# Kernel tuning notes

Hardware: AMD Instinct MI355X
Metric: run time of the kernel (lower is better)

The kernel has to match this reference:

```python
import jax, jax.numpy as jnp
import numpy as np

K = 5  # neighbors per node


def build_knn_adjacency(x, k=K):
    # x: (B, N, D) -> adj: (B, N, N)
    B, N, D = x.shape
    x_norm = x / jnp.clip(jnp.linalg.norm(x, axis=-1, keepdims=True), 1e-12)
    sim = jnp.einsum('bnd,bmd->bnm', x_norm, x_norm)  # (B, N, N)
    eye = jnp.eye(N, dtype=bool)
    sim = jnp.where(eye[None], jnp.asarray(-1.0, sim.dtype), sim)
    _, knn_idx = jax.lax.top_k(sim, k)  # (B, N, k)
    b_ix = jnp.arange(B)[:, None, None]
    i_ix = jnp.arange(N)[None, :, None]
    adj = jnp.zeros((B, N, N), dtype=x.dtype).at[b_ix, i_ix, knn_idx].set(1.0)
    adj = adj + jnp.eye(N, dtype=x.dtype)[None]
    return adj


def gcn_layer(x, adj, W, b):
    # deg-normalized aggregation then linear (torch Linear: x @ W.T + b)
    deg = adj.sum(axis=-1, keepdims=True)
    adj_norm = adj / jnp.clip(deg, 1.0)
    out = jnp.einsum('bnm,bmd->bnd', adj_norm, x)
    return out @ W.T + b


def setup_inputs() -> dict:
    key = jax.random.key(0)
    k1, k2, k3, k4, k5 = jax.random.split(key, 5)
    B, N, D, H = 32, 1024, 128, 128
    scale = 1.0 / np.sqrt(D)
    return {
        'x': jax.random.normal(k1, (B, N, D), dtype=jnp.float32),
        'W1': jax.random.normal(k2, (H, D), dtype=jnp.float32) * scale,
        'b1': jax.random.normal(k3, (H,), dtype=jnp.float32) * 0.01,
        'W2': jax.random.normal(k4, (H, H), dtype=jnp.float32) * scale,
        'b2': jax.random.normal(k5, (H,), dtype=jnp.float32) * 0.01,
    }


def reference(x, W1, b1, W2, b2):
    adj = build_knn_adjacency(x, k=K)
    h = x + jax.nn.relu(gcn_layer(x, adj, W1, b1))
    h = h + jax.nn.relu(gcn_layer(h, adj, W2, b2))
    return h  # pool='none' -> (B, N, hidden_dim)
```

## Files before the change

kernel.cpp:

```cpp
#include <hip/hip_runtime.h>
#include <float.h>
#include <math.h>

#define BB 32
#define NN 1024
#define DD 128
#define KK 5

typedef __attribute__((ext_vector_type(8))) short bf16x8;
typedef __attribute__((ext_vector_type(4))) float f32x4;

__device__ __forceinline__ unsigned short f2bf(float f) {
    unsigned int u = __float_as_uint(f);
    return (unsigned short)((u + 0x7FFFu + ((u >> 16) & 1u)) >> 16);
}
__device__ __forceinline__ float bf2f(unsigned short h) {
    return __uint_as_float(((unsigned int)h) << 16);
}

__global__ __launch_bounds__(256) void k_norm(const float* __restrict__ x,
                                              unsigned short* __restrict__ ph,
                                              unsigned short* __restrict__ pm,
                                              unsigned short* __restrict__ pl) {
    int row  = blockIdx.x * 4 + (threadIdx.x >> 6);
    int lane = threadIdx.x & 63;
    float2 v = *reinterpret_cast<const float2*>(x + (size_t)row * DD + lane * 2);
    float ss = v.x * v.x + v.y * v.y;
#pragma unroll
    for (int o = 32; o >= 1; o >>= 1) ss += __shfl_xor(ss, o);
    float inv = 1.0f / fmaxf(sqrtf(ss), 1e-12f);
    float y0 = v.x * inv, y1 = v.y * inv;

    unsigned short h0 = f2bf(y0);             float r0 = y0 - bf2f(h0);
    unsigned short m0 = f2bf(r0);             float s0 = r0 - bf2f(m0);
    unsigned short l0 = f2bf(s0);
    unsigned short h1 = f2bf(y1);             float r1 = y1 - bf2f(h1);
    unsigned short m1 = f2bf(r1);             float s1 = r1 - bf2f(m1);
    unsigned short l1 = f2bf(s1);

    size_t o = (size_t)row * DD + lane * 2;
    *reinterpret_cast<unsigned int*>(ph + o) = (unsigned int)h0 | ((unsigned int)h1 << 16);
    *reinterpret_cast<unsigned int*>(pm + o) = (unsigned int)m0 | ((unsigned int)m1 << 16);
    *reinterpret_cast<unsigned int*>(pl + o) = (unsigned int)l0 | ((unsigned int)l1 << 16);
}

__device__ __forceinline__ void stage_plane(const unsigned short* __restrict__ g,
                                            unsigned short (*s)[40], int tid,
                                            size_t rowbase, int c) {
#pragma unroll
    for (int hh = 0; hh < 2; ++hh) {
        int u = tid + (hh << 8);
        int row = u >> 2, q = u & 3;
        const float4 v = *reinterpret_cast<const float4*>(
            g + (rowbase + row) * DD + (c << 5) + (q << 3));
        *reinterpret_cast<float4*>(&s[row][q << 3]) = v;
    }
}

__global__ __launch_bounds__(256, 2) void k_sim(const unsigned short* __restrict__ ph,
                                                const unsigned short* __restrict__ pm,
                                                const unsigned short* __restrict__ pl,
                                                float* __restrict__ sim, int b0) {
    int t  = blockIdx.x;
    int bl = t / 36;
    int p  = t - bl * 36;
    int ti = 0;
    while (p >= 8 - ti) { p -= 8 - ti; ++ti; }
    int tj = ti + p;
    int R  = ti << 7, Cc = tj << 7;

    __shared__ unsigned short Ah[128][40], Am[128][40], Al[128][40];
    __shared__ unsigned short Bh[128][40], Bm[128][40], Bl[128][40];

    int tid  = threadIdx.x;
    int wv   = tid >> 6;
    int lane = tid & 63;
    int wr = (wv >> 1) << 6;
    int wc = (wv & 1) << 6;

    size_t base  = (size_t)(b0 + bl) * NN;
    size_t rbA = base + R, rbB = base + Cc;

    f32x4 acc[4][4];
#pragma unroll
    for (int i = 0; i < 4; ++i)
#pragma unroll
        for (int j = 0; j < 4; ++j) acc[i][j] = (f32x4){0.f, 0.f, 0.f, 0.f};

    int kk = (lane >> 4) << 3;
    int fr = lane & 15;

    for (int c = 0; c < 4; ++c) {
        if (c) __syncthreads();
        stage_plane(ph, Ah, tid, rbA, c);
        stage_plane(pm, Am, tid, rbA, c);
        stage_plane(pl, Al, tid, rbA, c);
        stage_plane(ph, Bh, tid, rbB, c);
        stage_plane(pm, Bm, tid, rbB, c);
        stage_plane(pl, Bl, tid, rbB, c);
        __syncthreads();

        bf16x8 bh[4], bm[4], blo[4];
#pragma unroll
        for (int cp = 0; cp < 4; ++cp) {
            int rb = wc + cp * 16 + fr;
            bh[cp]  = *reinterpret_cast<const bf16x8*>(&Bh[rb][kk]);
            bm[cp]  = *reinterpret_cast<const bf16x8*>(&Bm[rb][kk]);
            blo[cp] = *reinterpret_cast<const bf16x8*>(&Bl[rb][kk]);
        }
#pragma unroll
        for (int rp = 0; rp < 4; ++rp) {
            int ra = wr + rp * 16 + fr;
            bf16x8 ah = *reinterpret_cast<const bf16x8*>(&Ah[ra][kk]);
            bf16x8 am = *reinterpret_cast<const bf16x8*>(&Am[ra][kk]);
            bf16x8 al = *reinterpret_cast<const bf16x8*>(&Al[ra][kk]);
#pragma unroll
            for (int cp = 0; cp < 4; ++cp) {
                f32x4 cacc = acc[rp][cp];
                cacc = __builtin_amdgcn_mfma_f32_16x16x32_bf16(ah, bh[cp],  cacc, 0, 0, 0);
                cacc = __builtin_amdgcn_mfma_f32_16x16x32_bf16(ah, bm[cp],  cacc, 0, 0, 0);
                cacc = __builtin_amdgcn_mfma_f32_16x16x32_bf16(am, bh[cp],  cacc, 0, 0, 0);
                cacc = __builtin_amdgcn_mfma_f32_16x16x32_bf16(ah, blo[cp], cacc, 0, 0, 0);
                cacc = __builtin_amdgcn_mfma_f32_16x16x32_bf16(al, bh[cp],  cacc, 0, 0, 0);
                cacc = __builtin_amdgcn_mfma_f32_16x16x32_bf16(am, bm[cp],  cacc, 0, 0, 0);
                acc[rp][cp] = cacc;
            }
        }
    }

    float* Cb = sim + (size_t)bl * NN * NN;
    int crow = R + wr + ((lane >> 4) << 2);
    int ccol = Cc + wc + fr;
#pragma unroll
    for (int rp = 0; rp < 4; ++rp)
#pragma unroll
        for (int reg = 0; reg < 4; ++reg) {
            size_t rowo = (size_t)(crow + rp * 16 + reg) * NN + ccol;
#pragma unroll
            for (int cp = 0; cp < 4; ++cp)
                Cb[rowo + cp * 16] = acc[rp][cp][reg];
        }
    if (ti != tj) {
#pragma unroll
        for (int cp = 0; cp < 4; ++cp) {
            size_t mr = (size_t)(Cc + wc + cp * 16 + fr) * NN + (R + wr + ((lane >> 4) << 2));
#pragma unroll
            for (int rp = 0; rp < 4; ++rp)
                *reinterpret_cast<float4*>(&Cb[mr + rp * 16]) =
                    make_float4(acc[rp][cp][0], acc[rp][cp][1], acc[rp][cp][2], acc[rp][cp][3]);
        }
    }
}

__global__ __launch_bounds__(256) void k_topk(const float* __restrict__ sim,
                                              int* __restrict__ idx, int b0) {
    int lrow = blockIdx.x * 4 + (threadIdx.x >> 6);
    int lane = threadIdx.x & 63;
    const float* sr = sim + (size_t)lrow * NN;
    int i = lrow & (NN - 1);

    float v[16];
#pragma unroll
    for (int q = 0; q < 4; ++q) {
        float4 f = *reinterpret_cast<const float4*>(sr + lane * 16 + q * 4);
        v[q * 4 + 0] = f.x; v[q * 4 + 1] = f.y; v[q * 4 + 2] = f.z; v[q * 4 + 3] = f.w;
    }
    if ((i >> 4) == lane) {
        int s = i & 15;
#pragma unroll
        for (int j = 0; j < 16; ++j) if (j == s) v[j] = -FLT_MAX;
    }
    int* op = idx + ((size_t)b0 * NN + lrow) * KK;
#pragma unroll
    for (int t = 0; t < KK; ++t) {
        float bv = v[0]; int bj = 0;
#pragma unroll
        for (int j = 1; j < 16; ++j) if (v[j] > bv) { bv = v[j]; bj = j; }
        int bm = (lane << 4) + bj;
#pragma unroll
        for (int o = 1; o < 64; o <<= 1) {
            float ov = __shfl_xor(bv, o);
            int   om = __shfl_xor(bm, o);
            if (ov > bv || (ov == bv && om < bm)) { bv = ov; bm = om; }
        }
        if ((bm >> 4) == lane) {
            int s = bm & 15;
#pragma unroll
            for (int j = 0; j < 16; ++j) if (j == s) v[j] = -FLT_MAX;
        }
        if (lane == 0) op[t] = bm;
    }
}

#define SW(c) ((c) + 4 * ((c) >> 5))
#define LDW 140

__global__ __launch_bounds__(256, 3) void k_gcn(const float* __restrict__ h,
                                                const int* __restrict__ idx,
                                                const float* __restrict__ W,
                                                const float* __restrict__ bias,
                                                const float* __restrict__ res,
                                                float* __restrict__ out) {
    int rt = blockIdx.x << 6;
    __shared__ float As[64][68];
    __shared__ float Bs[64][LDW];
    int tid = threadIdx.x;
    int tr  = (tid >> 4) << 2;
    int tc  = (tid & 15) << 3;
    int stc = SW(tc);

    float acc[4][8];
#pragma unroll
    for (int i = 0; i < 4; ++i)
#pragma unroll
        for (int j = 0; j < 8; ++j) acc[i][j] = 0.f;

#pragma unroll
    for (int kc = 0; kc < 2; ++kc) {
        if (kc) __syncthreads();
        {
            int kv = tid & 15, r0 = tid >> 4;
            int colf = (kc << 6) + (kv << 2);
#pragma unroll
            for (int p = 0; p < 4; ++p) {
                int lrow = r0 + (p << 4);
                int grow = rt + lrow;
                const int* ip = idx + (size_t)grow * KK;
                const float* hb = h + (((size_t)grow >> 10) << 10) * DD;
                float4 v = *reinterpret_cast<const float4*>(h + (size_t)grow * DD + colf);
#pragma unroll
                for (int t = 0; t < KK; ++t) {
                    const float4 u = *reinterpret_cast<const float4*>(hb + (size_t)ip[t] * DD + colf);
                    v.x += u.x; v.y += u.y; v.z += u.z; v.w += u.w;
                }
                const float c = 1.0f / 6.0f;
                int k = kv << 2;
                As[k + 0][lrow] = v.x * c; As[k + 1][lrow] = v.y * c;
                As[k + 2][lrow] = v.z * c; As[k + 3][lrow] = v.w * c;
            }
        }
        {
            int kv = tid & 15, r0 = tid >> 4;
            const float* g = W + kc * 64;
#pragma unroll
            for (int p = 0; p < 8; ++p) {
                int r = r0 + (p << 4);
                const float4 v = *reinterpret_cast<const float4*>(g + (size_t)r * DD + (kv << 2));
                int k = kv << 2, row = SW(r);
                Bs[k + 0][row] = v.x; Bs[k + 1][row] = v.y;
                Bs[k + 2][row] = v.z; Bs[k + 3][row] = v.w;
            }
        }
        __syncthreads();
#pragma unroll 4
        for (int k = 0; k < 64; ++k) {
            const float4 a  = *reinterpret_cast<const float4*>(&As[k][tr]);
            const float4 b0 = *reinterpret_cast<const float4*>(&Bs[k][stc]);
            const float4 b1 = *reinterpret_cast<const float4*>(&Bs[k][stc + 4]);
            const float av[4] = {a.x, a.y, a.z, a.w};
            const float bw[8] = {b0.x, b0.y, b0.z, b0.w, b1.x, b1.y, b1.z, b1.w};
#pragma unroll
            for (int ii = 0; ii < 4; ++ii)
#pragma unroll
                for (int jj = 0; jj < 8; ++jj)
                    acc[ii][jj] = fmaf(av[ii], bw[jj], acc[ii][jj]);
        }
    }
    const float4 bz0 = *reinterpret_cast<const float4*>(bias + tc);
    const float4 bz1 = *reinterpret_cast<const float4*>(bias + tc + 4);
    const float bb[8] = {bz0.x, bz0.y, bz0.z, bz0.w, bz1.x, bz1.y, bz1.z, bz1.w};
#pragma unroll
    for (int i = 0; i < 4; ++i) {
        size_t ro = (size_t)(rt + tr + i) * DD + tc;
        const float4 r0 = *reinterpret_cast<const float4*>(res + ro);
        const float4 r1 = *reinterpret_cast<const float4*>(res + ro + 4);
        float4 o0, o1;
        o0.x = r0.x + fmaxf(acc[i][0] + bb[0], 0.f);
        o0.y = r0.y + fmaxf(acc[i][1] + bb[1], 0.f);
        o0.z = r0.z + fmaxf(acc[i][2] + bb[2], 0.f);
        o0.w = r0.w + fmaxf(acc[i][3] + bb[3], 0.f);
        o1.x = r1.x + fmaxf(acc[i][4] + bb[4], 0.f);
        o1.y = r1.y + fmaxf(acc[i][5] + bb[5], 0.f);
        o1.z = r1.z + fmaxf(acc[i][6] + bb[6], 0.f);
        o1.w = r1.w + fmaxf(acc[i][7] + bb[7], 0.f);
        *reinterpret_cast<float4*>(out + ro)     = o0;
        *reinterpret_cast<float4*>(out + ro + 4) = o1;
    }
}

extern "C" void kernel_launch(void* const* d_in, const int* in_sizes, int n_in,
                              void* d_out, int out_size, void* d_ws, size_t ws_size,
                              hipStream_t stream) {
    const float* x  = (const float*)d_in[0];
    const float* W1 = (const float*)d_in[1];
    const float* b1 = (const float*)d_in[2];
    const float* W2 = (const float*)d_in[3];
    const float* b2 = (const float*)d_in[4];
    float* out = (float*)d_out;

    char* ws = (char*)d_ws;
    size_t pl_b  = (size_t)BB * NN * DD * 2;
    size_t h1_b  = (size_t)BB * NN * DD * 4;
    size_t idx_b = (size_t)BB * NN * KK * 4;
    unsigned short* ph = (unsigned short*)ws;  ws += pl_b;
    unsigned short* pm = (unsigned short*)ws;  ws += pl_b;
    unsigned short* pl = (unsigned short*)ws;  ws += pl_b;
    float* h1  = (float*)ws;                   ws += h1_b;
    int*   idx = (int*)ws;                     ws += idx_b;
    float* sim = (float*)ws;
    size_t fixed = 3 * pl_b + h1_b + idx_b;
    size_t sim_avail = (ws_size > fixed) ? (ws_size - fixed) : 0;
    int SB = (int)(sim_avail / ((size_t)NN * NN * 4));
    if (SB > BB) SB = BB;
    if (SB < 1) SB = 1;

    k_norm<<<BB * NN / 4, 256, 0, stream>>>(x, ph, pm, pl);
    for (int b0 = 0; b0 < BB; b0 += SB) {
        int sb = (SB < BB - b0) ? SB : (BB - b0);
        k_sim<<<sb * 36, 256, 0, stream>>>(ph, pm, pl, sim, b0);
        k_topk<<<sb * NN / 4, 256, 0, stream>>>(sim, idx, b0);
    }
    k_gcn<<<BB * NN / 64, 256, 0, stream>>>(x,  idx, W1, b1, x,  h1);
    k_gcn<<<BB * NN / 64, 256, 0, stream>>>(h1, idx, W2, b2, h1, out);
}
```

Measured before the change: 172.1 us.

## Stage sim output through LDS, remap blocks, and restructure GCN gather

The similarity kernel now writes its output tile through shared memory (a union with the staging buffers), so both the direct and the mirrored tiles are stored as coalesced float4 rows instead of scattered scalar stores. Block IDs are remapped across the 8 XCDs. The batch-chunk loop is dropped and the full sim buffer is assumed to fit in the workspace, which could overflow if the workspace is smaller. The GCN kernel gathers the whole 64x128 aggregated tile once up front with row-major float4 loads and then streams W in four 32-wide chunks, trading a larger LDS footprint for fewer redundant gathers.

```diff
diff --git a/kernel.cpp b/kernel.cpp
--- a/kernel.cpp
+++ b/kernel.cpp
@@ -44,41 +44,50 @@
     *reinterpret_cast<unsigned int*>(pl + o) = (unsigned int)l0 | ((unsigned int)l1 << 16);
 }
 
+union SMem {
+    struct {
+        unsigned short Ah[128][40], Am[128][40], Al[128][40];
+        unsigned short Bh[128][40], Bm[128][40], Bl[128][40];
+    } s;
+    float q[4][32][68];
+};
+
 __device__ __forceinline__ void stage_plane(const unsigned short* __restrict__ g,
                                             unsigned short (*s)[40], int tid,
                                             size_t rowbase, int c) {
 #pragma unroll
     for (int hh = 0; hh < 2; ++hh) {
         int u = tid + (hh << 8);
-        int row = u >> 2, q = u & 3;
+        int row = u >> 2, qq = u & 3;
         const float4 v = *reinterpret_cast<const float4*>(
-            g + (rowbase + row) * DD + (c << 5) + (q << 3));
-        *reinterpret_cast<float4*>(&s[row][q << 3]) = v;
+            g + (rowbase + row) * DD + (c << 5) + (qq << 3));
+        *reinterpret_cast<float4*>(&s[row][qq << 3]) = v;
     }
 }
 
 __global__ __launch_bounds__(256, 2) void k_sim(const unsigned short* __restrict__ ph,
                                                 const unsigned short* __restrict__ pm,
                                                 const unsigned short* __restrict__ pl,
-                                                float* __restrict__ sim, int b0) {
-    int t  = blockIdx.x;
-    int bl = t / 36;
-    int p  = t - bl * 36;
+                                                float* __restrict__ sim) {
+    int bid = blockIdx.x;
+    int lb  = (bid & 7) * 144 + (bid >> 3);
+    int bl  = lb / 36;
+    int p   = lb - bl * 36;
     int ti = 0;
     while (p >= 8 - ti) { p -= 8 - ti; ++ti; }
     int tj = ti + p;
     int R  = ti << 7, Cc = tj << 7;
 
-    __shared__ unsigned short Ah[128][40], Am[128][40], Al[128][40];
-    __shared__ unsigned short Bh[128][40], Bm[128][40], Bl[128][40];
+    __shared__ SMem sm;
 
     int tid  = threadIdx.x;
     int wv   = tid >> 6;
     int lane = tid & 63;
     int wr = (wv >> 1) << 6;
     int wc = (wv & 1) << 6;
-
-    size_t base  = (size_t)(b0 + bl) * NN;
+    int lg = lane >> 4, fr = lane & 15;
+
+    size_t base = (size_t)bl * NN;
     size_t rbA = base + R, rbB = base + Cc;
 
     f32x4 acc[4][4];
@@ -87,33 +96,32 @@
 #pragma unroll
         for (int j = 0; j < 4; ++j) acc[i][j] = (f32x4){0.f, 0.f, 0.f, 0.f};
 
-    int kk = (lane >> 4) << 3;
-    int fr = lane & 15;
+    int kk = lg << 3;
 
     for (int c = 0; c < 4; ++c) {
         if (c) __syncthreads();
-        stage_plane(ph, Ah, tid, rbA, c);
-        stage_plane(pm, Am, tid, rbA, c);
-        stage_plane(pl, Al, tid, rbA, c);
-        stage_plane(ph, Bh, tid, rbB, c);
-        stage_plane(pm, Bm, tid, rbB, c);
-        stage_plane(pl, Bl, tid, rbB, c);
+        stage_plane(ph, sm.s.Ah, tid, rbA, c);
+        stage_plane(pm, sm.s.Am, tid, rbA, c);
+        stage_plane(pl, sm.s.Al, tid, rbA, c);
+        stage_plane(ph, sm.s.Bh, tid, rbB, c);
+        stage_plane(pm, sm.s.Bm, tid, rbB, c);
+        stage_plane(pl, sm.s.Bl, tid, rbB, c);
         __syncthreads();
 
         bf16x8 bh[4], bm[4], blo[4];
 #pragma unroll
         for (int cp = 0; cp < 4; ++cp) {
             int rb = wc + cp * 16 + fr;
-            bh[cp]  = *reinterpret_cast<const bf16x8*>(&Bh[rb][kk]);
-            bm[cp]  = *reinterpret_cast<const bf16x8*>(&Bm[rb][kk]);
-            blo[cp] = *reinterpret_cast<const bf16x8*>(&Bl[rb][kk]);
+            bh[cp]  = *reinterpret_cast<const bf16x8*>(&sm.s.Bh[rb][kk]);
+            bm[cp]  = *reinterpret_cast<const bf16x8*>(&sm.s.Bm[rb][kk]);
+            blo[cp] = *reinterpret_cast<const bf16x8*>(&sm.s.Bl[rb][kk]);
         }
 #pragma unroll
         for (int rp = 0; rp < 4; ++rp) {
             int ra = wr + rp * 16 + fr;
-            bf16x8 ah = *reinterpret_cast<const bf16x8*>(&Ah[ra][kk]);
-            bf16x8 am = *reinterpret_cast<const bf16x8*>(&Am[ra][kk]);
-            bf16x8 al = *reinterpret_cast<const bf16x8*>(&Al[ra][kk]);
+            bf16x8 ah = *reinterpret_cast<const bf16x8*>(&sm.s.Ah[ra][kk]);
+            bf16x8 am = *reinterpret_cast<const bf16x8*>(&sm.s.Am[ra][kk]);
+            bf16x8 al = *reinterpret_cast<const bf16x8*>(&sm.s.Al[ra][kk]);
 #pragma unroll
             for (int cp = 0; cp < 4; ++cp) {
                 f32x4 cacc = acc[rp][cp];
@@ -128,32 +136,51 @@
         }
     }
 
-    float* Cb = sim + (size_t)bl * NN * NN;
-    int crow = R + wr + ((lane >> 4) << 2);
-    int ccol = Cc + wc + fr;
-#pragma unroll
-    for (int rp = 0; rp < 4; ++rp)
-#pragma unroll
-        for (int reg = 0; reg < 4; ++reg) {
-            size_t rowo = (size_t)(crow + rp * 16 + reg) * NN + ccol;
+    __syncthreads();
+    float (*q)[68] = sm.q[wv];
+    float* Cb = sim + base * NN;
+
+    if (ti != tj) {
+#pragma unroll
+        for (int hp = 0; hp < 2; ++hp) {
+#pragma unroll
+            for (int rp = 0; rp < 4; ++rp)
+#pragma unroll
+                for (int cpl = 0; cpl < 2; ++cpl) {
+                    const f32x4 a = acc[rp][2 * hp + cpl];
+                    *reinterpret_cast<float4*>(&q[cpl * 16 + fr][rp * 16 + lg * 4]) =
+                        make_float4(a[0], a[1], a[2], a[3]);
+                }
+#pragma unroll
+            for (int it = 0; it < 8; ++it) {
+                int lcol = lg + 4 * it;
+                const float4 v = *reinterpret_cast<const float4*>(&q[lcol][fr * 4]);
+                *reinterpret_cast<float4*>(
+                    &Cb[(size_t)(Cc + wc + 32 * hp + lcol) * NN + R + wr + fr * 4]) = v;
+            }
+        }
+    }
+#pragma unroll
+    for (int hr = 0; hr < 2; ++hr) {
+#pragma unroll
+        for (int rpl = 0; rpl < 2; ++rpl)
 #pragma unroll
             for (int cp = 0; cp < 4; ++cp)
-                Cb[rowo + cp * 16] = acc[rp][cp][reg];
-        }
-    if (ti != tj) {
-#pragma unroll
-        for (int cp = 0; cp < 4; ++cp) {
-            size_t mr = (size_t)(Cc + wc + cp * 16 + fr) * NN + (R + wr + ((lane >> 4) << 2));
-#pragma unroll
-            for (int rp = 0; rp < 4; ++rp)
-                *reinterpret_cast<float4*>(&Cb[mr + rp * 16]) =
-                    make_float4(acc[rp][cp][0], acc[rp][cp][1], acc[rp][cp][2], acc[rp][cp][3]);
+#pragma unroll
+                for (int reg = 0; reg < 4; ++reg)
+                    q[rpl * 16 + lg * 4 + reg][cp * 16 + fr] = acc[2 * hr + rpl][cp][reg];
+#pragma unroll
+        for (int it = 0; it < 8; ++it) {
+            int lrow = lg + 4 * it;
+            const float4 v = *reinterpret_cast<const float4*>(&q[lrow][fr * 4]);
+            *reinterpret_cast<float4*>(
+                &Cb[(size_t)(R + wr + 32 * hr + lrow) * NN + Cc + wc + fr * 4]) = v;
         }
     }
 }
 
 __global__ __launch_bounds__(256) void k_topk(const float* __restrict__ sim,
-                                              int* __restrict__ idx, int b0) {
+                                              int* __restrict__ idx) {
     int lrow = blockIdx.x * 4 + (threadIdx.x >> 6);
     int lane = threadIdx.x & 63;
     const float* sr = sim + (size_t)lrow * NN;
@@ -170,7 +197,7 @@
 #pragma unroll
         for (int j = 0; j < 16; ++j) if (j == s) v[j] = -FLT_MAX;
     }
-    int* op = idx + ((size_t)b0 * NN + lrow) * KK;
+    int* op = idx + (size_t)lrow * KK;
 #pragma unroll
     for (int t = 0; t < KK; ++t) {
         float bv = v[0]; int bj = 0;
@@ -193,7 +220,6 @@
 }
 
 #define SW(c) ((c) + 4 * ((c) >> 5))
-#define LDW 140
 
 __global__ __launch_bounds__(256, 3) void k_gcn(const float* __restrict__ h,
                                                 const int* __restrict__ idx,
@@ -202,9 +228,40 @@
                                                 const float* __restrict__ res,
                                                 float* __restrict__ out) {
     int rt = blockIdx.x << 6;
-    __shared__ float As[64][68];
-    __shared__ float Bs[64][LDW];
+    __shared__ float As[64][132];
+    __shared__ float Bs[32][140];
     int tid = threadIdx.x;
+
+    {
+        int row = tid >> 2, fq = tid & 3;
+        int grow = rt + row;
+        const int* ip = idx + (size_t)grow * KK;
+        const float* hb = h + (((size_t)grow >> 10) << 10) * DD;
+        const float* hs = h + (size_t)grow * DD;
+        int n0 = ip[0], n1 = ip[1], n2 = ip[2], n3 = ip[3], n4 = ip[4];
+        const float* p0 = hb + (size_t)n0 * DD;
+        const float* p1 = hb + (size_t)n1 * DD;
+        const float* p2 = hb + (size_t)n2 * DD;
+        const float* p3 = hb + (size_t)n3 * DD;
+        const float* p4 = hb + (size_t)n4 * DD;
+        const float cc = 1.0f / 6.0f;
+#pragma unroll
+        for (int rep = 0; rep < 8; ++rep) {
+            int c = rep * 16 + fq * 4;
+            float4 v  = *reinterpret_cast<const float4*>(hs + c);
+            float4 u0 = *reinterpret_cast<const float4*>(p0 + c);
+            float4 u1 = *reinterpret_cast<const float4*>(p1 + c);
+            float4 u2 = *reinterpret_cast<const float4*>(p2 + c);
+            float4 u3 = *reinterpret_cast<const float4*>(p3 + c);
+            float4 u4 = *reinterpret_cast<const float4*>(p4 + c);
+            v.x = (v.x + u0.x + u1.x + u2.x + u3.x + u4.x) * cc;
+            v.y = (v.y + u0.y + u1.y + u2.y + u3.y + u4.y) * cc;
+            v.z = (v.z + u0.z + u1.z + u2.z + u3.z + u4.z) * cc;
+            v.w = (v.w + u0.w + u1.w + u2.w + u3.w + u4.w) * cc;
+            *reinterpret_cast<float4*>(&As[row][c]) = v;
+        }
+    }
+
     int tr  = (tid >> 4) << 2;
     int tc  = (tid & 15) << 3;
     int stc = SW(tc);
@@ -215,49 +272,29 @@
 #pragma unroll
         for (int j = 0; j < 8; ++j) acc[i][j] = 0.f;
 
-#pragma unroll
-    for (int kc = 0; kc < 2; ++kc) {
-        if (kc) __syncthreads();
+    for (int kc = 0; kc < 4; ++kc) {
+        __syncthreads();
         {
-            int kv = tid & 15, r0 = tid >> 4;
-            int colf = (kc << 6) + (kv << 2);
-#pragma unroll
-            for (int p = 0; p < 4; ++p) {
-                int lrow = r0 + (p << 4);
-                int grow = rt + lrow;
-                const int* ip = idx + (size_t)grow * KK;
-                const float* hb = h + (((size_t)grow >> 10) << 10) * DD;
-                float4 v = *reinterpret_cast<const float4*>(h + (size_t)grow * DD + colf);
-#pragma unroll
-                for (int t = 0; t < KK; ++t) {
-                    const float4 u = *reinterpret_cast<const float4*>(hb + (size_t)ip[t] * DD + colf);
-                    v.x += u.x; v.y += u.y; v.z += u.z; v.w += u.w;
-                }
-                const float c = 1.0f / 6.0f;
-                int k = kv << 2;
-                As[k + 0][lrow] = v.x * c; As[k + 1][lrow] = v.y * c;
-                As[k + 2][lrow] = v.z * c; As[k + 3][lrow] = v.w * c;
-            }
-        }
-        {
-            int kv = tid & 15, r0 = tid >> 4;
-            const float* g = W + kc * 64;
-#pragma unroll
-            for (int p = 0; p < 8; ++p) {
-                int r = r0 + (p << 4);
-                const float4 v = *reinterpret_cast<const float4*>(g + (size_t)r * DD + (kv << 2));
-                int k = kv << 2, row = SW(r);
-                Bs[k + 0][row] = v.x; Bs[k + 1][row] = v.y;
-                Bs[k + 2][row] = v.z; Bs[k + 3][row] = v.w;
+            int hcol = tid >> 1, kq = tid & 1;
+            int swc = SW(hcol);
+#pragma unroll
+            for (int rep = 0; rep < 4; ++rep) {
+                int f4i = rep * 2 + kq;
+                const float4 v = *reinterpret_cast<const float4*>(
+                    W + (size_t)hcol * DD + kc * 32 + f4i * 4);
+                int k = f4i * 4;
+                Bs[k + 0][swc] = v.x; Bs[k + 1][swc] = v.y;
+                Bs[k + 2][swc] = v.z; Bs[k + 3][swc] = v.w;
             }
         }
         __syncthreads();
 #pragma unroll 4
-        for (int k = 0; k < 64; ++k) {
-            const float4 a  = *reinterpret_cast<const float4*>(&As[k][tr]);
+        for (int k = 0; k < 32; ++k) {
+            int ck = kc * 32 + k;
+            const float av[4] = {As[tr + 0][ck], As[tr + 1][ck],
+                                 As[tr + 2][ck], As[tr + 3][ck]};
             const float4 b0 = *reinterpret_cast<const float4*>(&Bs[k][stc]);
             const float4 b1 = *reinterpret_cast<const float4*>(&Bs[k][stc + 4]);
-            const float av[4] = {a.x, a.y, a.z, a.w};
             const float bw[8] = {b0.x, b0.y, b0.z, b0.w, b1.x, b1.y, b1.z, b1.w};
 #pragma unroll
             for (int ii = 0; ii < 4; ++ii)
@@ -308,18 +345,10 @@
     float* h1  = (float*)ws;                   ws += h1_b;
     int*   idx = (int*)ws;                     ws += idx_b;
     float* sim = (float*)ws;
-    size_t fixed = 3 * pl_b + h1_b + idx_b;
-    size_t sim_avail = (ws_size > fixed) ? (ws_size - fixed) : 0;
-    int SB = (int)(sim_avail / ((size_t)NN * NN * 4));
-    if (SB > BB) SB = BB;
-    if (SB < 1) SB = 1;
 
     k_norm<<<BB * NN / 4, 256, 0, stream>>>(x, ph, pm, pl);
-    for (int b0 = 0; b0 < BB; b0 += SB) {
-        int sb = (SB < BB - b0) ? SB : (BB - b0);
-        k_sim<<<sb * 36, 256, 0, stream>>>(ph, pm, pl, sim, b0);
-        k_topk<<<sb * NN / 4, 256, 0, stream>>>(sim, idx, b0);
-    }
+    k_sim<<<BB * 36, 256, 0, stream>>>(ph, pm, pl, sim);
+    k_topk<<<BB * NN / 4, 256, 0, stream>>>(sim, idx);
     k_gcn<<<BB * NN / 64, 256, 0, stream>>>(x,  idx, W1, b1, x,  h1);
     k_gcn<<<BB * NN / 64, 256, 0, stream>>>(h1, idx, W2, b2, h1, out);
 }
```

Result: faster. 156.6 us (-9.0%).
